# Kernel tuning notes

Measured on AMD Instinct MI355X. Metric: run time of the kernel, lower is better.

Reference implementation:

```python
import jax, jax.numpy as jnp
import numpy as np

BS, T, N, E = 4, 6, 400, 3000
D = 100        # object_dim == state_dim == out_fts (forced by code)
NS = 30        # num states
NOBJ = 300     # object vocab
NET = 10       # n edge types
NSTEPS = 3     # GatedGraphConv n_steps


def setup_inputs() -> dict:
    key = jax.random.key(0)
    ks = jax.random.split(key, 16)
    def nrm(k, shape, s=0.05):
        return jax.random.normal(k, shape, jnp.float32) * s
    return dict(
        class_names=jax.random.randint(ks[0], (BS, T, N), 0, NOBJ),
        states=jax.random.uniform(ks[1], (BS, T, N, NS), jnp.float32),
        edges=jax.random.randint(ks[2], (BS, T, E, 2), 0, N),
        edge_types=jax.random.randint(ks[3], (BS, T, E), 0, NET),
        visibility=jax.random.uniform(ks[4], (BS, T, N), jnp.float32),
        mask_edges=jnp.ones((BS, T, E), jnp.float32),
        obj_emb=nrm(ks[5], (NOBJ, D)),
        state_W=nrm(ks[6], (D, NS)), state_b=jnp.zeros((D,), jnp.float32),
        c1_W=nrm(ks[7], (D, 2 * D)), c1_b=jnp.zeros((D,), jnp.float32),
        c2_W=nrm(ks[8], (D, D)), c2_b=jnp.zeros((D,), jnp.float32),
        edge_embed=nrm(ks[9], (NET, D * D)),
        g_wih=nrm(ks[10], (3 * D, D)), g_whh=nrm(ks[11], (3 * D, D)),
        g_bih=jnp.zeros((3 * D,), jnp.float32), g_bhh=jnp.zeros((3 * D,), jnp.float32),
        o_wih=nrm(ks[12], (3 * D, D)), o_whh=nrm(ks[13], (3 * D, D)),
    )


def _gru(x, h, wih, whh, bih=None, bhh=None):
    # torch.nn.GRUCell semantics
    gi = x @ wih.T
    gh = h @ whh.T
    if bih is not None:
        gi = gi + bih
        gh = gh + bhh
    ir, iz, inn = jnp.split(gi, 3, axis=-1)
    hr, hz, hn = jnp.split(gh, 3, axis=-1)
    r = jax.nn.sigmoid(ir + hr)
    z = jax.nn.sigmoid(iz + hz)
    n = jnp.tanh(inn + r * hn)
    return (1.0 - z) * n + z * h


def reference(class_names, states, edges, edge_types, visibility, mask_edges,
              obj_emb, state_W, state_b, c1_W, c1_b, c2_W, c2_b,
              edge_embed, g_wih, g_whh, g_bih, g_bhh, o_wih, o_whh):
    bs, t_len, n = class_names.shape
    # initial node representation (ClassNameStateRepresentation)
    emb = obj_emb[class_names]                       # [bs,T,N,D]
    st = states @ state_W.T + state_b                # [bs,T,N,D]
    x = jnp.concatenate([emb, st], -1)
    x = jax.nn.relu(x @ c1_W.T + c1_b) @ c2_W.T + c2_b  # [bs,T,N,D]

    off = (jnp.arange(bs) * n)[:, None]              # flatten batch into node axis
    h = jnp.zeros((bs * n, D), x.dtype)              # outer temporal GRU state
    reprs = []
    for t in range(t_len):
        h = _gru(x[:, t].reshape(bs * n, D), h, o_wih, o_whh)  # bias=False
        feat_flat = h                                 # [bs*N, D]
        src = (edges[:, t, :, 0] + off).reshape(-1)   # [bs*E]
        dst = (edges[:, t, :, 1] + off).reshape(-1)
        # per-edge DxD matrices, masked (as in original)
        W = edge_embed[edge_types[:, t].reshape(-1)].reshape(-1, D, D)
        W = W * mask_edges[:, t].reshape(-1)[:, None, None]
        # NOTE: original never updates feat_flat inside the n_steps loop,
        # so every step reads the same source features; we replicate that.
        feat_out = feat_flat
        for _ in range(NSTEPS):
            msg = jnp.einsum('eij,ej->ei', W, feat_flat[src])           # per-edge matvec
            a = jax.ops.segment_sum(msg, dst, num_segments=bs * n)     # scatter-add
            feat_out = _gru(a, feat_flat, g_wih, g_whh, g_bih, g_bhh)
        reprs.append(feat_out.reshape(bs, n, D) * visibility[:, t, :, None])
    node_reprs = jnp.stack(reprs, 1)                  # [bs,T,N,D]
    num_nodes = visibility.sum(-1) + 1e-9             # [bs,T]
    global_repr = (node_reprs * visibility[..., None]).sum(2) / num_nodes[..., None]
    return node_reprs, global_repr
```

## Files before the change

### kernel.cpp

```cpp
#include <hip/hip_runtime.h>

#define BSZ   4
#define TT    6
#define NNODE 400
#define EED   3000
#define DDIM  100
#define NSDIM 30
#define NETYP 10
#define BN    (BSZ*NNODE)
#define NROW  (BSZ*TT*NNODE)
#define NEDGE (BSZ*TT*EED)
#define KPAD  1024

#define OFF_PRE1 0
#define OFF_QT   30000
#define OFF_BQ   33000
#define OFF_BF   33104
#define OFF_WIT  33408
#define OFF_BI   63408
#define OFF_BH   63744
#define OFF_WFH  64080
#define OFF_WFL  85584
#define OFF_WOH  107088
#define OFF_WOL  128592
#define OFF_BWF  150096
#define OFF_BWPK 450096
#define OFF_WHPK 622128
#define OFF_HALL 643632
#define OFF_START 1603632
#define OFF_SE   1613236
#define OFF_INV  1757248
#define OFF_GI   1757280

typedef __attribute__((ext_vector_type(8))) short bf16x8;
typedef __attribute__((ext_vector_type(4))) float f32x4;

__device__ __forceinline__ float sigf(float v) { return 1.0f / (1.0f + expf(-v)); }

__device__ __forceinline__ short bfc(float f) {
    union { float f; unsigned u; } v; v.f = f;
    unsigned r = v.u + 0x7fffu + ((v.u >> 16) & 1u);
    return (short)(r >> 16);
}

__device__ __forceinline__ float bf2f(short h) {
    union { unsigned u; float f; } x; x.u = ((unsigned)(unsigned short)h) << 16;
    return x.f;
}

__device__ __forceinline__ unsigned cvtpk(float lo, float hi) {
    unsigned r;
    asm("v_cvt_pk_bf16_f32 %0, %1, %2" : "=v"(r) : "v"(lo), "v"(hi));
    return r;
}

__global__ __launch_bounds__(256) void k_front(
    const float* __restrict__ obj_emb, const float* __restrict__ c1_W,
    const float* __restrict__ c1_b, const float* __restrict__ state_W,
    const float* __restrict__ state_b, const float* __restrict__ c2_W,
    const float* __restrict__ c2_b, const float* __restrict__ o_wih,
    const float* __restrict__ o_whh, const float* __restrict__ g_wih,
    const float* __restrict__ g_bih, const float* __restrict__ g_bhh,
    const float* __restrict__ vis, const int* __restrict__ edges,
    const int* __restrict__ etype, const float* __restrict__ emask,
    float* __restrict__ pre1, float* __restrict__ QT, float* __restrict__ bQ,
    float* __restrict__ bfold, float* __restrict__ WiT,
    float* __restrict__ bI, float* __restrict__ bH,
    ushort* __restrict__ WFH, ushort* __restrict__ WFL,
    ushort* __restrict__ WOH, ushort* __restrict__ WOL,
    float* __restrict__ inv_nv, float* __restrict__ gout,
    int* __restrict__ start, int2* __restrict__ sortedE2) {
    int tid = threadIdx.x;
    if (blockIdx.x < 24) {
        __shared__ int hcnt[400];
        __shared__ int hstart[400];
        int c = blockIdx.x;
        int t = c >> 2, b = c & 3;
        int febase = (b * TT + t) * EED;
        for (int i = tid; i < 400; i += 256) hcnt[i] = 0;
        __syncthreads();
        for (int i = tid; i < EED; i += 256)
            atomicAdd(&hcnt[edges[(febase + i) * 2 + 1]], 1);
        __syncthreads();
        if (tid < 64) {
            int lane = tid, carry = 0;
            for (int ch = 0; ch < 7; ++ch) {
                int idx = ch * 64 + lane;
                int orig = (idx < 400) ? hcnt[idx] : 0;
                int v = orig;
                #pragma unroll
                for (int off = 1; off < 64; off <<= 1) {
                    int u = __shfl_up(v, off, 64);
                    if (lane >= off) v += u;
                }
                if (idx < 400) hstart[idx] = carry + (v - orig);
                carry += __shfl(v, 63, 64);
            }
        }
        __syncthreads();
        for (int i = tid; i < 400; i += 256) {
            start[c * 400 + i] = c * EED + hstart[i];
            hcnt[i] = hstart[i];
        }
        if (c == 23 && tid == 0) start[NROW] = NEDGE;
        __syncthreads();
        for (int i = tid; i < EED; i += 256) {
            int fe = febase + i;
            int2 ed = *(const int2*)(edges + fe * 2);
            int pos = atomicAdd(&hcnt[ed.y], 1);
            int g = etype[fe];
            float m = emask[fe];
            sortedE2[c * EED + pos] = make_int2(ed.x | (g << 16), __float_as_int(m));
        }
        return;
    }
    int i = (blockIdx.x - 24) * 256 + tid;
    if (i < 30000) {
        int cls = i / DDIM, d1 = i % DDIM;
        float acc = 0.f;
        for (int k = 0; k < DDIM; ++k)
            acc += obj_emb[cls * DDIM + k] * c1_W[d1 * 2 * DDIM + k];
        pre1[i] = acc;
    } else if (i < 33000) {
        int j = i - 30000, s = j / DDIM, d1 = j % DDIM;
        float acc = 0.f;
        for (int d = 0; d < DDIM; ++d)
            acc += c1_W[d1 * 2 * DDIM + DDIM + d] * state_W[d * NSDIM + s];
        QT[j] = acc;
    } else if (i < 33100) {
        int d1 = i - 33000;
        float acc = c1_b[d1];
        for (int d = 0; d < DDIM; ++d)
            acc += state_b[d] * c1_W[d1 * 2 * DDIM + DDIM + d];
        bQ[d1] = acc;
    } else if (i < 33400) {
        int o = i - 33100;
        float acc = 0.f;
        for (int d = 0; d < DDIM; ++d)
            acc += o_wih[o * DDIM + d] * c2_b[d];
        bfold[o] = acc;
    } else if (i < 76408) {
        int e = i - 33400;
        int j = e & 7, frag = e >> 3;
        int l = frag & 63, ct = (frag >> 6) % 21, kt = frag / (21 * 64);
        int col = ct * 16 + (l & 15);
        int gate = col / 112, dd = col % 112;
        int k = kt * 32 + ((l >> 4) << 3) + j;
        float v = 0.f;
        if (k < DDIM && dd < DDIM) {
            int o = gate * DDIM + dd;
            for (int d = 0; d < DDIM; ++d)
                v += o_wih[o * DDIM + d] * c2_W[d * DDIM + k];
        }
        short hi = bfc(v);
        WFH[frag * 8 + j] = (ushort)hi;
        WFL[frag * 8 + j] = (ushort)bfc(v - bf2f(hi));
    } else if (i < 119416) {
        int e = i - 76408;
        int j = e & 7, frag = e >> 3;
        int l = frag & 63, ct = (frag >> 6) % 21, kt = frag / (21 * 64);
        int col = ct * 16 + (l & 15);
        int gate = col / 112, dd = col % 112;
        int k = kt * 32 + ((l >> 4) << 3) + j;
        float v = 0.f;
        if (k < DDIM && dd < DDIM)
            v = o_whh[(gate * DDIM + dd) * DDIM + k];
        short hi = bfc(v);
        WOH[frag * 8 + j] = (ushort)hi;
        WOL[frag * 8 + j] = (ushort)bfc(v - bf2f(hi));
    } else if (i < 149416) {
        int j = i - 119416, k = j / 300, o = j % 300;
        WiT[j] = g_wih[o * DDIM + k];
    } else if (i < 149752) {
        int col = i - 149416, gate = col / 112, o = col % 112;
        bI[col] = (o < DDIM) ? g_bih[gate * DDIM + o] : 0.f;
    } else if (i < 150088) {
        int col = i - 149752, gate = col / 112, o = col % 112;
        bH[col] = (o < DDIM) ? g_bhh[gate * DDIM + o] : 0.f;
    } else if (i >= 150144 && i < 151680) {
        int g = (i - 150144) >> 6;
        int lane = i & 63;
        float s = 0.f;
        for (int n = lane; n < NNODE; n += 64)
            s += vis[g * NNODE + n];
        #pragma unroll
        for (int off = 32; off > 0; off >>= 1)
            s += __shfl_down(s, off, 64);
        if (lane == 0) inv_nv[g] = 1.f / (s + 1e-9f);
    } else if (i >= 151680 && i < 154080) {
        gout[i - 151680] = 0.f;
    }
}

__global__ __launch_bounds__(448) void k_mid(
    const float* __restrict__ edge_embed, const float* __restrict__ WiT,
    float* __restrict__ BW,
    const int* __restrict__ cls, const float* __restrict__ states,
    const float* __restrict__ pre1, const float* __restrict__ QT,
    const float* __restrict__ bQ, const float* __restrict__ bfold,
    const bf16x8* __restrict__ WFH, const bf16x8* __restrict__ WFL,
    float* __restrict__ GI) {
    __shared__ float st_lds[16 * NSDIM];
    __shared__ float hid_lds[16 * 112];
    __shared__ int cls_lds[16];
    int tid = threadIdx.x;
    if (blockIdx.x < 670) {
        int i = blockIdx.x * 448 + tid;
        if (i < 1000 * 300) {
            int kk = i / 300, go = i % 300;
            int g = kk / DDIM, k = kk % DDIM;
            const float* es = edge_embed + g * DDIM * DDIM + k;
            float acc = 0.f;
            for (int j = 0; j < DDIM; ++j)
                acc += es[j * DDIM] * WiT[j * 300 + go];
            BW[i] = acc;
        }
        return;
    }
    int r0 = (blockIdx.x - 670) * 16;
    for (int idx = tid; idx < 16 * NSDIM; idx += 448) st_lds[idx] = states[r0 * NSDIM + idx];
    if (tid < 16) cls_lds[tid] = cls[r0 + tid];
    __syncthreads();
    #pragma unroll
    for (int u = 0; u < 4; ++u) {
        int it = tid + u * 448;
        if (it < 1600) {
            int n = it / 100, d = it % 100;
            float acc = bQ[d] + pre1[cls_lds[n] * DDIM + d];
            for (int s = 0; s < NSDIM; ++s)
                acc += QT[s * DDIM + d] * st_lds[n * NSDIM + s];
            hid_lds[n * 112 + d] = fmaxf(acc, 0.f);
        }
    }
    __syncthreads();
    int w = tid >> 6, l = tid & 63, rit = l & 15, kgrp = l >> 4;
    f32x4 acc3[3];
    acc3[0] = acc3[1] = acc3[2] = (f32x4){0.f, 0.f, 0.f, 0.f};
    for (int kt = 0; kt < 4; ++kt) {
        bf16x8 Ahi, Alo;
        #pragma unroll
        for (int j = 0; j < 8; ++j) {
            int k = kt * 32 + kgrp * 8 + j;
            float v = (k < DDIM) ? hid_lds[rit * 112 + k] : 0.f;
            short hi = bfc(v);
            Ahi[j] = hi;
            Alo[j] = bfc(v - bf2f(hi));
        }
        #pragma unroll
        for (int p = 0; p < 3; ++p) {
            int ct = w + p * 7;
            bf16x8 Bhi = WFH[(kt * 21 + ct) * 64 + l];
            bf16x8 Blo = WFL[(kt * 21 + ct) * 64 + l];
            acc3[p] = __builtin_amdgcn_mfma_f32_16x16x32_bf16(Ahi, Bhi, acc3[p], 0, 0, 0);
            acc3[p] = __builtin_amdgcn_mfma_f32_16x16x32_bf16(Alo, Bhi, acc3[p], 0, 0, 0);
            acc3[p] = __builtin_amdgcn_mfma_f32_16x16x32_bf16(Ahi, Blo, acc3[p], 0, 0, 0);
        }
    }
    int dd = w * 16 + rit;
    if (dd < DDIM) {
        int b = r0 / (TT * NNODE), t = (r0 / NNODE) % TT, nn0 = r0 % NNODE;
        int trow0 = t * BN + b * NNODE + nn0;
        #pragma unroll
        for (int p = 0; p < 3; ++p) {
            float bias = bfold[p * DDIM + dd];
            #pragma unroll
            for (int j = 0; j < 4; ++j) {
                int row = kgrp * 4 + j;
                GI[(trow0 + row) * 336 + p * 112 + dd] = acc3[p][j] + bias;
            }
        }
    }
}

__global__ __launch_bounds__(448) void k_mid2(const float* __restrict__ GI,
    const bf16x8* __restrict__ WOH, const bf16x8* __restrict__ WOL,
    float* __restrict__ Hall,
    const float* __restrict__ BW, const float* __restrict__ g_whh,
    bf16x8* __restrict__ BWpk, bf16x8* __restrict__ WHpk) {
    __shared__ float h_lds[16 * 112];
    int tid = threadIdx.x;
    if (blockIdx.x >= 100) {
        int i = (blockIdx.x - 100) * 448 + tid;
        if (i < 43008) {
            int l = i & 63, c = (i >> 6) % 21, kt = i / (21 * 64);
            int col = c * 16 + (l & 15);
            int gate = col / 112, o = col % 112;
            bf16x8 r;
            #pragma unroll
            for (int j = 0; j < 8; ++j) {
                int kk = kt * 32 + ((l >> 4) << 3) + j;
                float v = (kk < 1000 && o < DDIM) ? BW[kk * 300 + gate * DDIM + o] : 0.f;
                r[j] = bfc(v);
            }
            BWpk[i] = r;
        } else if (i < 48384) {
            int id = i - 43008;
            int l = id & 63, c = (id >> 6) % 21, kt2 = id / (21 * 64);
            int col = c * 16 + (l & 15);
            int gate = col / 112, o = col % 112;
            bf16x8 r;
            #pragma unroll
            for (int j = 0; j < 8; ++j) {
                int k = kt2 * 32 + ((l >> 4) << 3) + j;
                float v = (k < DDIM && o < DDIM) ? g_whh[(gate * DDIM + o) * DDIM + k] : 0.f;
                r[j] = bfc(v);
            }
            WHpk[id] = r;
        }
        return;
    }
    int bn0 = blockIdx.x * 16;
    for (int idx = tid; idx < 16 * 112; idx += 448) h_lds[idx] = 0.f;
    __syncthreads();
    int w = tid >> 6, l = tid & 63, rit = l & 15, kgrp = l >> 4;
    int dd = w * 16 + rit;
    for (int t = 0; t < TT; ++t) {
        float gir[4], giz[4], gin[4], hold[4];
        if (dd < DDIM) {
            #pragma unroll
            for (int j = 0; j < 4; ++j) {
                int node = kgrp * 4 + j;
                int trow = t * BN + bn0 + node;
                gir[j] = GI[trow * 336 + dd];
                giz[j] = GI[trow * 336 + 112 + dd];
                gin[j] = GI[trow * 336 + 224 + dd];
                hold[j] = h_lds[node * 112 + dd];
            }
        }
        f32x4 a0 = (f32x4){0.f, 0.f, 0.f, 0.f};
        f32x4 a1 = (f32x4){0.f, 0.f, 0.f, 0.f};
        f32x4 a2 = (f32x4){0.f, 0.f, 0.f, 0.f};
        if (t > 0) {
            for (int kt = 0; kt < 4; ++kt) {
                bf16x8 Ahi, Alo;
                #pragma unroll
                for (int j = 0; j < 8; ++j) {
                    int k = kt * 32 + kgrp * 8 + j;
                    float v = (k < DDIM) ? h_lds[rit * 112 + k] : 0.f;
                    short hi = bfc(v);
                    Ahi[j] = hi;
                    Alo[j] = bfc(v - bf2f(hi));
                }
                {
                    bf16x8 Bhi = WOH[(kt * 21 + w) * 64 + l];
                    bf16x8 Blo = WOL[(kt * 21 + w) * 64 + l];
                    a0 = __builtin_amdgcn_mfma_f32_16x16x32_bf16(Ahi, Bhi, a0, 0, 0, 0);
                    a0 = __builtin_amdgcn_mfma_f32_16x16x32_bf16(Alo, Bhi, a0, 0, 0, 0);
                    a0 = __builtin_amdgcn_mfma_f32_16x16x32_bf16(Ahi, Blo, a0, 0, 0, 0);
                }
                {
                    bf16x8 Bhi = WOH[(kt * 21 + w + 7) * 64 + l];
                    bf16x8 Blo = WOL[(kt * 21 + w + 7) * 64 + l];
                    a1 = __builtin_amdgcn_mfma_f32_16x16x32_bf16(Ahi, Bhi, a1, 0, 0, 0);
                    a1 = __builtin_amdgcn_mfma_f32_16x16x32_bf16(Alo, Bhi, a1, 0, 0, 0);
                    a1 = __builtin_amdgcn_mfma_f32_16x16x32_bf16(Ahi, Blo, a1, 0, 0, 0);
                }
                {
                    bf16x8 Bhi = WOH[(kt * 21 + w + 14) * 64 + l];
                    bf16x8 Blo = WOL[(kt * 21 + w + 14) * 64 + l];
                    a2 = __builtin_amdgcn_mfma_f32_16x16x32_bf16(Ahi, Bhi, a2, 0, 0, 0);
                    a2 = __builtin_amdgcn_mfma_f32_16x16x32_bf16(Alo, Bhi, a2, 0, 0, 0);
                    a2 = __builtin_amdgcn_mfma_f32_16x16x32_bf16(Ahi, Blo, a2, 0, 0, 0);
                }
            }
        }
        __syncthreads();
        if (dd < DDIM) {
            #pragma unroll
            for (int j = 0; j < 4; ++j) {
                int node = kgrp * 4 + j;
                int trow = t * BN + bn0 + node;
                float r = sigf(gir[j] + a0[j]);
                float z = sigf(giz[j] + a1[j]);
                float nn = tanhf(gin[j] + r * a2[j]);
                float hnew = (1.f - z) * nn + z * hold[j];
                h_lds[node * 112 + dd] = hnew;
                Hall[trow * DDIM + dd] = hnew;
            }
        }
        __syncthreads();
    }
}

__global__ __launch_bounds__(448) void k_fused16(
    const int* __restrict__ start, const int2* __restrict__ sortedE2,
    const bf16x8* __restrict__ BWpk, const bf16x8* __restrict__ WHpk,
    const float* __restrict__ bI, const float* __restrict__ bH,
    const float* __restrict__ Hall, const float* __restrict__ visv,
    const float* __restrict__ inv_nv, float* __restrict__ out,
    float* __restrict__ gout) {
    __shared__ unsigned lds[8192];
    int tid = threadIdx.x;
    int w = tid >> 6, l = tid & 63;
    int rit = l & 15, kgrp = l >> 4;
    int rbase = blockIdx.x * 16;

    for (int r = w; r < 16; r += 7) {
        int trd = rbase + r;
        int s0 = start[trd], s1 = start[trd + 1];
        int rowbase = (trd / NNODE) * NNODE;
        float acc[16];
        #pragma unroll
        for (int j = 0; j < 16; ++j) acc[j] = 0.f;
        for (int e0 = s0; e0 < s1; e0 += 4) {
            float2 hA[4], hB[4];
            float me[4];
            int ge[4];
            #pragma unroll
            for (int e = 0; e < 4; ++e) {
                int idx = e0 + e;
                int2 rec = (idx < s1) ? sortedE2[idx] : make_int2(0, 0);
                int src = rec.x & 0xffff;
                int g = rec.x >> 16;
                ge[e] = g;
                me[e] = __int_as_float(rec.y);
                const float* hs = Hall + (size_t)(rowbase + src) * DDIM;
                int k0 = g * 100;
                int J0 = k0 >> 7, J1 = (k0 + 99) >> 7;
                int sA = 128 * J0 + 2 * l, sB = 128 * J1 + 2 * l;
                bool aA = (sA >= k0) && (sA < k0 + 100);
                bool aB = (J1 != J0) && (sB >= k0) && (sB < k0 + 100);
                hA[e] = aA ? *(const float2*)(hs + (sA - k0)) : make_float2(0.f, 0.f);
                hB[e] = aB ? *(const float2*)(hs + (sB - k0)) : make_float2(0.f, 0.f);
            }
            #pragma unroll
            for (int e = 0; e < 4; ++e) {
                float m = me[e];
                float ax = m * hA[e].x, ay = m * hA[e].y;
                float bx = m * hB[e].x, by = m * hB[e].y;
                switch (ge[e]) {
                    case 0: acc[0] += ax; acc[1] += ay; break;
                    case 1: acc[0] += ax; acc[1] += ay; acc[2] += bx; acc[3] += by; break;
                    case 2: acc[2] += ax; acc[3] += ay; acc[4] += bx; acc[5] += by; break;
                    case 3: acc[4] += ax; acc[5] += ay; acc[6] += bx; acc[7] += by; break;
                    case 4: acc[6] += ax; acc[7] += ay; break;
                    case 5: acc[6] += ax; acc[7] += ay; acc[8] += bx; acc[9] += by; break;
                    case 6: acc[8] += ax; acc[9] += ay; acc[10] += bx; acc[11] += by; break;
                    case 7: acc[10] += ax; acc[11] += ay; acc[12] += bx; acc[13] += by; break;
                    case 8: acc[12] += ax; acc[13] += ay; acc[14] += bx; acc[15] += by; break;
                    case 9: acc[14] += ax; acc[15] += ay; break;
                }
            }
        }
        #pragma unroll
        for (int j = 0; j < 8; ++j) {
            unsigned word = cvtpk(acc[2 * j], acc[2 * j + 1]);
            int g16 = 16 * j + (l >> 2);
            int wd = r * 512 + ((g16 * 4) ^ ((r & 7) << 2)) + (l & 3);
            lds[wd] = word;
        }
    }
    __syncthreads();

    f32x4 acc[3];
    acc[0] = acc[1] = acc[2] = (f32x4){0.f, 0.f, 0.f, 0.f};

    for (int kt = 0; kt < 32; ++kt) {
        bf16x8 fb0 = BWpk[(kt * 21 + w) * 64 + l];
        bf16x8 fb1 = BWpk[(kt * 21 + w + 7) * 64 + l];
        bf16x8 fb2 = BWpk[(kt * 21 + w + 14) * 64 + l];
        int wd = rit * 512 + (((kt * 16 + kgrp * 4)) ^ ((rit & 7) << 2));
        bf16x8 fa = *(bf16x8*)&lds[wd];
        acc[0] = __builtin_amdgcn_mfma_f32_16x16x32_bf16(fa, fb0, acc[0], 0, 0, 0);
        acc[1] = __builtin_amdgcn_mfma_f32_16x16x32_bf16(fa, fb1, acc[1], 0, 0, 0);
        acc[2] = __builtin_amdgcn_mfma_f32_16x16x32_bf16(fa, fb2, acc[2], 0, 0, 0);
    }
    __syncthreads();

    for (int i = tid; i < 256; i += 448) {
        int row = i >> 4, g16 = i & 15;
        int k0 = g16 * 8;
        const float* hs = Hall + (size_t)(rbase + row) * DDIM;
        float v[8];
        #pragma unroll
        for (int jj = 0; jj < 8; ++jj)
            v[jj] = (k0 + jj < DDIM) ? hs[k0 + jj] : 0.f;
        int4 wv;
        wv.x = (int)cvtpk(v[0], v[1]);
        wv.y = (int)cvtpk(v[2], v[3]);
        wv.z = (int)cvtpk(v[4], v[5]);
        wv.w = (int)cvtpk(v[6], v[7]);
        int wd = row * 64 + ((g16 * 4) ^ ((row & 7) << 2));
        *(int4*)&lds[wd] = wv;
    }
    __syncthreads();

    f32x4 hacc = (f32x4){0.f, 0.f, 0.f, 0.f};
    for (int kt2 = 0; kt2 < 4; ++kt2) {
        bf16x8 fb0 = WHpk[(kt2 * 21 + w) * 64 + l];
        bf16x8 fb1 = WHpk[(kt2 * 21 + w + 7) * 64 + l];
        bf16x8 fb2 = WHpk[(kt2 * 21 + w + 14) * 64 + l];
        int wd = rit * 64 + (((kt2 * 16 + kgrp * 4)) ^ ((rit & 7) << 2));
        bf16x8 fh = *(bf16x8*)&lds[wd];
        acc[0] = __builtin_amdgcn_mfma_f32_16x16x32_bf16(fh, fb0, acc[0], 0, 0, 0);
        acc[1] = __builtin_amdgcn_mfma_f32_16x16x32_bf16(fh, fb1, acc[1], 0, 0, 0);
        hacc   = __builtin_amdgcn_mfma_f32_16x16x32_bf16(fh, fb2, hacc, 0, 0, 0);
    }

    int col = w * 16 + rit;
    if (col < DDIM) {
        float bIr = bI[col], bIz = bI[112 + col], bIn = bI[224 + col];
        float bHr = bH[col], bHz = bH[112 + col], bHn = bH[224 + col];
        int t = rbase / BN, r2 = rbase % BN, b = r2 / NNODE, n0 = r2 % NNODE;
        int bt = b * TT + t;
        int trow0 = rbase + kgrp * 4;
        int brow0 = bt * NNODE + n0 + kgrp * 4;
        float gs = 0.f;
        #pragma unroll
        for (int j = 0; j < 4; ++j) {
            float r = sigf(acc[0][j] + bIr + bHr);
            float z = sigf(acc[1][j] + bIz + bHz);
            float ghn = hacc[j] + bHn;
            float nn = tanhf(acc[2][j] + bIn + r * ghn);
            float hold = Hall[(trow0 + j) * DDIM + col];
            float feat = (1.f - z) * nn + z * hold;
            int brow = brow0 + j;
            float v = visv[brow];
            float outv = feat * v;
            out[brow * DDIM + col] = outv;
            gs += outv * v;
        }
        gs += __shfl_xor(gs, 16, 64);
        gs += __shfl_xor(gs, 32, 64);
        if (kgrp == 0)
            atomicAdd(&gout[bt * DDIM + col], gs * inv_nv[bt]);
    }
}

extern "C" void kernel_launch(void* const* d_in, const int* in_sizes, int n_in,
                              void* d_out, int out_size, void* d_ws, size_t ws_size,
                              hipStream_t stream) {
    const int*   class_names = (const int*)d_in[0];
    const float* states      = (const float*)d_in[1];
    const int*   edges       = (const int*)d_in[2];
    const int*   edge_types  = (const int*)d_in[3];
    const float* visibility  = (const float*)d_in[4];
    const float* mask_edges  = (const float*)d_in[5];
    const float* obj_emb     = (const float*)d_in[6];
    const float* state_W     = (const float*)d_in[7];
    const float* state_b     = (const float*)d_in[8];
    const float* c1_W        = (const float*)d_in[9];
    const float* c1_b        = (const float*)d_in[10];
    const float* c2_W        = (const float*)d_in[11];
    const float* c2_b        = (const float*)d_in[12];
    const float* edge_embed  = (const float*)d_in[13];
    const float* g_wih       = (const float*)d_in[14];
    const float* g_whh       = (const float*)d_in[15];
    const float* g_bih       = (const float*)d_in[16];
    const float* g_bhh       = (const float*)d_in[17];
    const float* o_wih       = (const float*)d_in[18];
    const float* o_whh       = (const float*)d_in[19];

    float* out = (float*)d_out;
    float* gout = out + (size_t)NROW * DDIM;
    float* ws  = (float*)d_ws;
    float*  pre1  = ws + OFF_PRE1;
    float*  QT    = ws + OFF_QT;
    float*  bQ    = ws + OFF_BQ;
    float*  bfold = ws + OFF_BF;
    float*  WiT   = ws + OFF_WIT;
    float*  bI    = ws + OFF_BI;
    float*  bH    = ws + OFF_BH;
    ushort* WFH   = (ushort*)(ws + OFF_WFH);
    ushort* WFL   = (ushort*)(ws + OFF_WFL);
    ushort* WOH   = (ushort*)(ws + OFF_WOH);
    ushort* WOL   = (ushort*)(ws + OFF_WOL);
    float*  BWf   = ws + OFF_BWF;
    bf16x8* BWpk  = (bf16x8*)(ws + OFF_BWPK);
    bf16x8* WHpk  = (bf16x8*)(ws + OFF_WHPK);
    float*  Hall  = ws + OFF_HALL;
    int*    start = (int*)(ws + OFF_START);
    int2*   sortedE2 = (int2*)(ws + OFF_SE);
    float*  inv_nv= ws + OFF_INV;
    float*  GI    = ws + OFF_GI;

    k_front<<<626, 256, 0, stream>>>(obj_emb, c1_W, c1_b, state_W, state_b,
                                     c2_W, c2_b, o_wih, o_whh, g_wih, g_bih, g_bhh,
                                     visibility, edges, edge_types, mask_edges,
                                     pre1, QT, bQ, bfold, WiT, bI, bH,
                                     WFH, WFL, WOH, WOL, inv_nv, gout,
                                     start, sortedE2);
    k_mid<<<1270, 448, 0, stream>>>(edge_embed, WiT, BWf, class_names, states,
                                    pre1, QT, bQ, bfold,
                                    (const bf16x8*)WFH, (const bf16x8*)WFL, GI);
    k_mid2<<<208, 448, 0, stream>>>(GI, (const bf16x8*)WOH, (const bf16x8*)WOL,
                                    Hall, BWf, g_whh, BWpk, WHpk);
    k_fused16<<<NROW / 16, 448, 0, stream>>>(start, sortedE2, BWpk, WHpk, bI, bH,
                                             Hall, visibility, inv_nv, out, gout);
}
```

Before: 118.1 us.

## Split edge gather into its own kernel and double GEMM rows per block

```diff
diff --git a/kernel.cpp b/kernel.cpp
--- a/kernel.cpp
+++ b/kernel.cpp
@@ -31,6 +31,7 @@
 #define OFF_SE   1613236
 #define OFF_INV  1757248
 #define OFF_GI   1757280
+#define OFF_UB   4982880
 
 typedef __attribute__((ext_vector_type(8))) short bf16x8;
 typedef __attribute__((ext_vector_type(4))) float f32x4;
@@ -382,92 +383,105 @@
     }
 }
 
-__global__ __launch_bounds__(448) void k_fused16(
+__global__ __launch_bounds__(256) void k_gather(
     const int* __restrict__ start, const int2* __restrict__ sortedE2,
+    const float* __restrict__ Hall, unsigned* __restrict__ Ub2) {
+    int gid = blockIdx.x * 256 + threadIdx.x;
+    int trd = gid >> 6, l = gid & 63;
+    int s0 = start[trd], s1 = start[trd + 1];
+    int rowbase = (trd / NNODE) * NNODE;
+    float acc[16];
+    #pragma unroll
+    for (int j = 0; j < 16; ++j) acc[j] = 0.f;
+    for (int e0 = s0; e0 < s1; e0 += 4) {
+        float2 hA[4], hB[4];
+        float me[4];
+        int ge[4];
+        #pragma unroll
+        for (int e = 0; e < 4; ++e) {
+            int idx = e0 + e;
+            int2 rec = (idx < s1) ? sortedE2[idx] : make_int2(0, 0);
+            int src = rec.x & 0xffff;
+            int g = rec.x >> 16;
+            ge[e] = g;
+            me[e] = __int_as_float(rec.y);
+            const float* hs = Hall + (size_t)(rowbase + src) * DDIM;
+            int k0 = g * 100;
+            int J0 = k0 >> 7, J1 = (k0 + 99) >> 7;
+            int sA = 128 * J0 + 2 * l, sB = 128 * J1 + 2 * l;
+            bool aA = (sA >= k0) && (sA < k0 + 100);
+            bool aB = (J1 != J0) && (sB >= k0) && (sB < k0 + 100);
+            hA[e] = aA ? *(const float2*)(hs + (sA - k0)) : make_float2(0.f, 0.f);
+            hB[e] = aB ? *(const float2*)(hs + (sB - k0)) : make_float2(0.f, 0.f);
+        }
+        #pragma unroll
+        for (int e = 0; e < 4; ++e) {
+            float m = me[e];
+            float ax = m * hA[e].x, ay = m * hA[e].y;
+            float bx = m * hB[e].x, by = m * hB[e].y;
+            switch (ge[e]) {
+                case 0: acc[0] += ax; acc[1] += ay; break;
+                case 1: acc[0] += ax; acc[1] += ay; acc[2] += bx; acc[3] += by; break;
+                case 2: acc[2] += ax; acc[3] += ay; acc[4] += bx; acc[5] += by; break;
+                case 3: acc[4] += ax; acc[5] += ay; acc[6] += bx; acc[7] += by; break;
+                case 4: acc[6] += ax; acc[7] += ay; break;
+                case 5: acc[6] += ax; acc[7] += ay; acc[8] += bx; acc[9] += by; break;
+                case 6: acc[8] += ax; acc[9] += ay; acc[10] += bx; acc[11] += by; break;
+                case 7: acc[10] += ax; acc[11] += ay; acc[12] += bx; acc[13] += by; break;
+                case 8: acc[12] += ax; acc[13] += ay; acc[14] += bx; acc[15] += by; break;
+                case 9: acc[14] += ax; acc[15] += ay; break;
+            }
+        }
+    }
+    unsigned* urow = Ub2 + (size_t)trd * 512;
+    #pragma unroll
+    for (int j = 0; j < 8; ++j)
+        urow[64 * j + l] = cvtpk(acc[2 * j], acc[2 * j + 1]);
+}
+
+__global__ __launch_bounds__(448) void k_fused32(const ushort* __restrict__ Ub,
     const bf16x8* __restrict__ BWpk, const bf16x8* __restrict__ WHpk,
     const float* __restrict__ bI, const float* __restrict__ bH,
     const float* __restrict__ Hall, const float* __restrict__ visv,
     const float* __restrict__ inv_nv, float* __restrict__ out,
     float* __restrict__ gout) {
-    __shared__ unsigned lds[8192];
+    __shared__ unsigned lds[16384];
     int tid = threadIdx.x;
     int w = tid >> 6, l = tid & 63;
     int rit = l & 15, kgrp = l >> 4;
-    int rbase = blockIdx.x * 16;
-
-    for (int r = w; r < 16; r += 7) {
-        int trd = rbase + r;
-        int s0 = start[trd], s1 = start[trd + 1];
-        int rowbase = (trd / NNODE) * NNODE;
-        float acc[16];
-        #pragma unroll
-        for (int j = 0; j < 16; ++j) acc[j] = 0.f;
-        for (int e0 = s0; e0 < s1; e0 += 4) {
-            float2 hA[4], hB[4];
-            float me[4];
-            int ge[4];
-            #pragma unroll
-            for (int e = 0; e < 4; ++e) {
-                int idx = e0 + e;
-                int2 rec = (idx < s1) ? sortedE2[idx] : make_int2(0, 0);
-                int src = rec.x & 0xffff;
-                int g = rec.x >> 16;
-                ge[e] = g;
-                me[e] = __int_as_float(rec.y);
-                const float* hs = Hall + (size_t)(rowbase + src) * DDIM;
-                int k0 = g * 100;
-                int J0 = k0 >> 7, J1 = (k0 + 99) >> 7;
-                int sA = 128 * J0 + 2 * l, sB = 128 * J1 + 2 * l;
-                bool aA = (sA >= k0) && (sA < k0 + 100);
-                bool aB = (J1 != J0) && (sB >= k0) && (sB < k0 + 100);
-                hA[e] = aA ? *(const float2*)(hs + (sA - k0)) : make_float2(0.f, 0.f);
-                hB[e] = aB ? *(const float2*)(hs + (sB - k0)) : make_float2(0.f, 0.f);
-            }
-            #pragma unroll
-            for (int e = 0; e < 4; ++e) {
-                float m = me[e];
-                float ax = m * hA[e].x, ay = m * hA[e].y;
-                float bx = m * hB[e].x, by = m * hB[e].y;
-                switch (ge[e]) {
-                    case 0: acc[0] += ax; acc[1] += ay; break;
-                    case 1: acc[0] += ax; acc[1] += ay; acc[2] += bx; acc[3] += by; break;
-                    case 2: acc[2] += ax; acc[3] += ay; acc[4] += bx; acc[5] += by; break;
-                    case 3: acc[4] += ax; acc[5] += ay; acc[6] += bx; acc[7] += by; break;
-                    case 4: acc[6] += ax; acc[7] += ay; break;
-                    case 5: acc[6] += ax; acc[7] += ay; acc[8] += bx; acc[9] += by; break;
-                    case 6: acc[8] += ax; acc[9] += ay; acc[10] += bx; acc[11] += by; break;
-                    case 7: acc[10] += ax; acc[11] += ay; acc[12] += bx; acc[13] += by; break;
-                    case 8: acc[12] += ax; acc[13] += ay; acc[14] += bx; acc[15] += by; break;
-                    case 9: acc[14] += ax; acc[15] += ay; break;
-                }
-            }
-        }
-        #pragma unroll
-        for (int j = 0; j < 8; ++j) {
-            unsigned word = cvtpk(acc[2 * j], acc[2 * j + 1]);
-            int g16 = 16 * j + (l >> 2);
-            int wd = r * 512 + ((g16 * 4) ^ ((r & 7) << 2)) + (l & 3);
-            lds[wd] = word;
-        }
+    int rbase = blockIdx.x * 32;
+
+    for (int i = tid; i < 4096; i += 448) {
+        int row = i >> 7, g16 = i & 127;
+        int4 wv = *(const int4*)(Ub + (size_t)(rbase + row) * KPAD + g16 * 8);
+        int wd = row * 512 + ((g16 * 4) ^ ((row & 7) << 2));
+        *(int4*)&lds[wd] = wv;
     }
     __syncthreads();
 
-    f32x4 acc[3];
-    acc[0] = acc[1] = acc[2] = (f32x4){0.f, 0.f, 0.f, 0.f};
+    f32x4 acc[2][3];
+    #pragma unroll
+    for (int mt = 0; mt < 2; ++mt)
+        #pragma unroll
+        for (int q = 0; q < 3; ++q) acc[mt][q] = (f32x4){0.f, 0.f, 0.f, 0.f};
 
     for (int kt = 0; kt < 32; ++kt) {
         bf16x8 fb0 = BWpk[(kt * 21 + w) * 64 + l];
         bf16x8 fb1 = BWpk[(kt * 21 + w + 7) * 64 + l];
         bf16x8 fb2 = BWpk[(kt * 21 + w + 14) * 64 + l];
-        int wd = rit * 512 + (((kt * 16 + kgrp * 4)) ^ ((rit & 7) << 2));
-        bf16x8 fa = *(bf16x8*)&lds[wd];
-        acc[0] = __builtin_amdgcn_mfma_f32_16x16x32_bf16(fa, fb0, acc[0], 0, 0, 0);
-        acc[1] = __builtin_amdgcn_mfma_f32_16x16x32_bf16(fa, fb1, acc[1], 0, 0, 0);
-        acc[2] = __builtin_amdgcn_mfma_f32_16x16x32_bf16(fa, fb2, acc[2], 0, 0, 0);
+        #pragma unroll
+        for (int mt = 0; mt < 2; ++mt) {
+            int row = mt * 16 + rit;
+            int wd = row * 512 + (((kt * 16 + kgrp * 4)) ^ ((row & 7) << 2));
+            bf16x8 fa = *(bf16x8*)&lds[wd];
+            acc[mt][0] = __builtin_amdgcn_mfma_f32_16x16x32_bf16(fa, fb0, acc[mt][0], 0, 0, 0);
+            acc[mt][1] = __builtin_amdgcn_mfma_f32_16x16x32_bf16(fa, fb1, acc[mt][1], 0, 0, 0);
+            acc[mt][2] = __builtin_amdgcn_mfma_f32_16x16x32_bf16(fa, fb2, acc[mt][2], 0, 0, 0);
+        }
     }
     __syncthreads();
 
-    for (int i = tid; i < 256; i += 448) {
+    for (int i = tid; i < 512; i += 448) {
         int row = i >> 4, g16 = i & 15;
         int k0 = g16 * 8;
         const float* hs = Hall + (size_t)(rbase + row) * DDIM;
@@ -485,45 +499,56 @@
     }
     __syncthreads();
 
-    f32x4 hacc = (f32x4){0.f, 0.f, 0.f, 0.f};
+    f32x4 hacc[2];
+    hacc[0] = (f32x4){0.f, 0.f, 0.f, 0.f};
+    hacc[1] = (f32x4){0.f, 0.f, 0.f, 0.f};
     for (int kt2 = 0; kt2 < 4; ++kt2) {
         bf16x8 fb0 = WHpk[(kt2 * 21 + w) * 64 + l];
         bf16x8 fb1 = WHpk[(kt2 * 21 + w + 7) * 64 + l];
         bf16x8 fb2 = WHpk[(kt2 * 21 + w + 14) * 64 + l];
-        int wd = rit * 64 + (((kt2 * 16 + kgrp * 4)) ^ ((rit & 7) << 2));
-        bf16x8 fh = *(bf16x8*)&lds[wd];
-        acc[0] = __builtin_amdgcn_mfma_f32_16x16x32_bf16(fh, fb0, acc[0], 0, 0, 0);
-        acc[1] = __builtin_amdgcn_mfma_f32_16x16x32_bf16(fh, fb1, acc[1], 0, 0, 0);
-        hacc   = __builtin_amdgcn_mfma_f32_16x16x32_bf16(fh, fb2, hacc, 0, 0, 0);
+        #pragma unroll
+        for (int mt = 0; mt < 2; ++mt) {
+            int row = mt * 16 + rit;
+            int wd = row * 64 + (((kt2 * 16 + kgrp * 4)) ^ ((row & 7) << 2));
+            bf16x8 fh = *(bf16x8*)&lds[wd];
+            acc[mt][0] = __builtin_amdgcn_mfma_f32_16x16x32_bf16(fh, fb0, acc[mt][0], 0, 0, 0);
+            acc[mt][1] = __builtin_amdgcn_mfma_f32_16x16x32_bf16(fh, fb1, acc[mt][1], 0, 0, 0);
+            hacc[mt]  = __builtin_amdgcn_mfma_f32_16x16x32_bf16(fh, fb2, hacc[mt], 0, 0, 0);
+        }
     }
 
     int col = w * 16 + rit;
     if (col < DDIM) {
         float bIr = bI[col], bIz = bI[112 + col], bIn = bI[224 + col];
         float bHr = bH[col], bHz = bH[112 + col], bHn = bH[224 + col];
-        int t = rbase / BN, r2 = rbase % BN, b = r2 / NNODE, n0 = r2 % NNODE;
-        int bt = b * TT + t;
-        int trow0 = rbase + kgrp * 4;
-        int brow0 = bt * NNODE + n0 + kgrp * 4;
-        float gs = 0.f;
-        #pragma unroll
-        for (int j = 0; j < 4; ++j) {
-            float r = sigf(acc[0][j] + bIr + bHr);
-            float z = sigf(acc[1][j] + bIz + bHz);
-            float ghn = hacc[j] + bHn;
-            float nn = tanhf(acc[2][j] + bIn + r * ghn);
-            float hold = Hall[(trow0 + j) * DDIM + col];
-            float feat = (1.f - z) * nn + z * hold;
-            int brow = brow0 + j;
-            float v = visv[brow];
-            float outv = feat * v;
-            out[brow * DDIM + col] = outv;
-            gs += outv * v;
-        }
-        gs += __shfl_xor(gs, 16, 64);
-        gs += __shfl_xor(gs, 32, 64);
-        if (kgrp == 0)
-            atomicAdd(&gout[bt * DDIM + col], gs * inv_nv[bt]);
+        int t = rbase / BN;
+        #pragma unroll
+        for (int mt = 0; mt < 2; ++mt) {
+            int r2 = (rbase + mt * 16) % BN;
+            int b = r2 / NNODE, n0 = r2 % NNODE;
+            int bt = b * TT + t;
+            int trow0 = rbase + mt * 16 + kgrp * 4;
+            int brow0 = bt * NNODE + n0 + kgrp * 4;
+            float gs = 0.f;
+            #pragma unroll
+            for (int j = 0; j < 4; ++j) {
+                float r = sigf(acc[mt][0][j] + bIr + bHr);
+                float z = sigf(acc[mt][1][j] + bIz + bHz);
+                float ghn = hacc[mt][j] + bHn;
+                float nn = tanhf(acc[mt][2][j] + bIn + r * ghn);
+                float hold = Hall[(trow0 + j) * DDIM + col];
+                float feat = (1.f - z) * nn + z * hold;
+                int brow = brow0 + j;
+                float v = visv[brow];
+                float outv = feat * v;
+                out[brow * DDIM + col] = outv;
+                gs += outv * v;
+            }
+            gs += __shfl_xor(gs, 16, 64);
+            gs += __shfl_xor(gs, 32, 64);
+            if (kgrp == 0)
+                atomicAdd(&gout[bt * DDIM + col], gs * inv_nv[bt]);
+        }
     }
 }
 
@@ -573,6 +598,7 @@
     int2*   sortedE2 = (int2*)(ws + OFF_SE);
     float*  inv_nv= ws + OFF_INV;
     float*  GI    = ws + OFF_GI;
+    ushort* Ub    = (ushort*)(ws + OFF_UB);
 
     k_front<<<626, 256, 0, stream>>>(obj_emb, c1_W, c1_b, state_W, state_b,
                                      c2_W, c2_b, o_wih, o_whh, g_wih, g_bih, g_bhh,
@@ -585,6 +611,7 @@
                                     (const bf16x8*)WFH, (const bf16x8*)WFL, GI);
     k_mid2<<<208, 448, 0, stream>>>(GI, (const bf16x8*)WOH, (const bf16x8*)WOL,
                                     Hall, BWf, g_whh, BWpk, WHpk);
-    k_fused16<<<NROW / 16, 448, 0, stream>>>(start, sortedE2, BWpk, WHpk, bI, bH,
-                                             Hall, visibility, inv_nv, out, gout);
-}
+    k_gather<<<NROW / 4, 256, 0, stream>>>(start, sortedE2, Hall, (unsigned*)Ub);
+    k_fused32<<<NROW / 32, 448, 0, stream>>>(Ub, BWpk, WHpk, bI, bH, Hall,
+                                             visibility, inv_nv, out, gout);
+}
```

Measured after the change: 104.6 us. 11.4% less time.
